# Kernel optimization log

Hardware: AMD Instinct MI355X
Metric: run time of the kernel (lower is better)

## Reference

```python
import jax, jax.numpy as jnp
import numpy as np

B, H, W, C = 8, 256, 256, 64
M1, M2 = 32, 32
SCALE = 1.0 / (C * C)


def setup_inputs() -> dict:
    key = jax.random.key(0)
    ku, k1, k2, k3, k4 = jax.random.split(key, 5)
    u = jax.random.normal(ku, (B, H, W, C), dtype=jnp.float32)
    wshape = (C, C, M1, M2)
    w_pos_r = SCALE * jax.random.normal(k1, wshape, dtype=jnp.float32)
    w_pos_i = SCALE * jax.random.normal(k2, wshape, dtype=jnp.float32)
    w_neg_r = SCALE * jax.random.normal(k3, wshape, dtype=jnp.float32)
    w_neg_i = SCALE * jax.random.normal(k4, wshape, dtype=jnp.float32)
    return {"u": u, "w_pos_r": w_pos_r, "w_pos_i": w_pos_i,
            "w_neg_r": w_neg_r, "w_neg_i": w_neg_i}


def _compl_mul2d(inp, weights):
    # inp: [B, m1, m2, Cin] complex; weights: [Cin, Cout, m1, m2] complex
    return jnp.einsum('bxyi,ioxy->bxyo', inp, weights)


def reference(u, w_pos_r, w_pos_i, w_neg_r, w_neg_i):
    b, h, w, c = u.shape
    wf = w // 2 + 1  # rfft size along W
    u_ft = jnp.fft.rfft2(u, axes=(1, 2))  # [B, H, Wf, C] complex
    w_pos = jax.lax.complex(w_pos_r, w_pos_i)
    w_neg = jax.lax.complex(w_neg_r, w_neg_i)
    top = _compl_mul2d(u_ft[:, :M1, :M2, :], w_pos)   # low positive freqs
    bot = _compl_mul2d(u_ft[:, h - M1:, :M2, :], w_neg)  # low negative freqs
    # out_ft zero-initialized, only truncated modes populated.
    # (Original allocates [B,H,W,C] but irfft2 with s=(H,W) only reads
    #  the first W//2+1 columns, which equals this [B,H,Wf,C] tensor.)
    out_ft = jnp.zeros((b, h, wf, c), dtype=u_ft.dtype)
    out_ft = out_ft.at[:, :M1, :M2, :].set(top)
    out_ft = out_ft.at[:, h - M1:, :M2, :].set(bot)
    # out_ft[:, -M1:M1] assignment in original is an empty slice (M1 <= H/2): no-op.
    return jnp.fft.irfft2(out_ft, s=(h, w), axes=(1, 2)).astype(u.dtype)
```

## Files before the change

kernel.cpp:

```cpp
#include <hip/hip_runtime.h>
#include <math.h>

#define BB 8
#define HH 256
#define WW 256
#define CC 64

__device__ inline void cmac(float2& a, float tx, float ty, float2 v) {
    a.x += tx * v.x - ty * v.y;
    a.y += tx * v.y + ty * v.x;
}

__global__ __launch_bounds__(256) void k_tw(float2* __restrict__ Tf,
                                            float2* __restrict__ Ti,
                                            float* __restrict__ Ty,
                                            float* __restrict__ T2) {
    int e = blockIdx.x * 256 + threadIdx.x;
    if (e < 16384) {
        int x = e >> 6;
        int j = e & 63;
        int kxa = j + ((j >> 5) * 192);
        int tt = (kxa * x) & 255;
        float ang = (float)tt * (6.283185307179586f / 256.0f);
        float s, c;
        sincosf(ang, &s, &c);
        Tf[(size_t)x * 64 + j] = make_float2(c, -s);
        const float k = 2.0f / 65536.0f;
        Ti[(size_t)j * 256 + x] = make_float2(c * k, s * k);
    } else {
        int f = e - 16384;
        if (f < 8192) {
            int yp = f >> 6;
            int col = f & 63;
            int par = (col >> 5) & 1;
            int cs = (col >> 4) & 1;
            int m = col & 15;
            int ky = 2 * m + par;
            int tt = (ky * yp) & 255;
            float ang = (float)tt * (6.283185307179586f / 256.0f);
            float s, c;
            sincosf(ang, &s, &c);
            Ty[f] = cs ? -s : c;
        } else {
            int g = f - 8192;
            int pi = g >> 12;
            int j = (g >> 7) & 31;
            int p = g & 127;
            int m = j >> 1, ri = j & 1;
            int ky = 2 * m + pi;
            int tt = (ky * p) & 255;
            float ang = (float)tt * (6.283185307179586f / 256.0f);
            float s, c;
            sincosf(ang, &s, &c);
            T2[g] = ri ? -s : c;
        }
    }
}

__global__ __launch_bounds__(256, 4) void k_fwd_y(const float* __restrict__ u,
                                                  const float* __restrict__ Ty,
                                                  float2* __restrict__ V) {
    __shared__ float ue[32 * 68];
    __shared__ float uo[32 * 68];
    __shared__ float Tt[32 * 68];

    int t = threadIdx.x;
    int b = blockIdx.x >> 8;
    int x = blockIdx.x & 255;
    int i4 = (t & 15) * 4;
    int w = t >> 4;
    int p = w & 1;
    int kyq = w >> 1;
    int yy = t >> 3;
    int c0 = (t & 7) * 8;

    const float* ub = u + ((size_t)(b * HH + x)) * (WW * CC);
    const float* uplane = p ? uo : ue;

    float ar0x=0,ar0y=0,ar0z=0,ar0w=0, ai0x=0,ai0y=0,ai0z=0,ai0w=0;
    float ar1x=0,ar1y=0,ar1z=0,ar1w=0, ai1x=0,ai1y=0,ai1z=0,ai1w=0;

    for (int yt = 0; yt < 4; ++yt) {
        const float* plo = ub + (size_t)(yt * 32 + yy) * CC + c0;
        const float* phi = plo + 128 * CC;
        float4 l0 = *(const float4*)(plo);
        float4 l1 = *(const float4*)(plo + 4);
        float4 h0 = *(const float4*)(phi);
        float4 h1 = *(const float4*)(phi + 4);
        const float* tsrc = Ty + (size_t)(yt * 32 + yy) * 64 + c0;
        float4 t0 = *(const float4*)(tsrc);
        float4 t1 = *(const float4*)(tsrc + 4);

        __syncthreads();
        int wb = yy * 68 + c0;
        *(float4*)(ue + wb)     = make_float4(l0.x + h0.x, l0.y + h0.y, l0.z + h0.z, l0.w + h0.w);
        *(float4*)(ue + wb + 4) = make_float4(l1.x + h1.x, l1.y + h1.y, l1.z + h1.z, l1.w + h1.w);
        *(float4*)(uo + wb)     = make_float4(l0.x - h0.x, l0.y - h0.y, l0.z - h0.z, l0.w - h0.w);
        *(float4*)(uo + wb + 4) = make_float4(l1.x - h1.x, l1.y - h1.y, l1.z - h1.z, l1.w - h1.w);
        *(float4*)(Tt + wb)     = t0;
        *(float4*)(Tt + wb + 4) = t1;
        __syncthreads();

        #pragma unroll
        for (int y2 = 0; y2 < 32; ++y2) {
            const float* tb = Tt + y2 * 68 + p * 32 + kyq * 2;
            float2 cp = *(const float2*)(tb);
            float2 sp = *(const float2*)(tb + 16);
            float4 uq = *(const float4*)(uplane + y2 * 68 + i4);
            ar0x += cp.x * uq.x; ar0y += cp.x * uq.y; ar0z += cp.x * uq.z; ar0w += cp.x * uq.w;
            ai0x += sp.x * uq.x; ai0y += sp.x * uq.y; ai0z += sp.x * uq.z; ai0w += sp.x * uq.w;
            ar1x += cp.y * uq.x; ar1y += cp.y * uq.y; ar1z += cp.y * uq.z; ar1w += cp.y * uq.w;
            ai1x += sp.y * uq.x; ai1y += sp.y * uq.y; ai1z += sp.y * uq.z; ai1w += sp.y * uq.w;
        }
    }

    {
        int ky = 4 * kyq + p;
        float2* vp = V + (size_t)(b * HH + x) * 2048 + ky * 64 + i4;
        *(float4*)(vp)     = make_float4(ar0x, ai0x, ar0y, ai0y);
        *(float4*)(vp + 2) = make_float4(ar0z, ai0z, ar0w, ai0w);
    }
    {
        int ky = 4 * kyq + 2 + p;
        float2* vp = V + (size_t)(b * HH + x) * 2048 + ky * 64 + i4;
        *(float4*)(vp)     = make_float4(ar1x, ai1x, ar1y, ai1y);
        *(float4*)(vp + 2) = make_float4(ar1z, ai1z, ar1w, ai1w);
    }
}

__global__ __launch_bounds__(256) void k_fwd_x(const float2* __restrict__ Tf,
                                               const float2* __restrict__ V,
                                               float2* __restrict__ U) {
    __shared__ float sRe[2 * 2048];
    __shared__ float sIm[2 * 2048];
    __shared__ float2 Ts[32 * 16];

    int bx = blockIdx.x;
    int jq = bx & 3;
    int ky = (bx >> 2) & 31;
    int b  = bx >> 7;
    int t = threadIdx.x;
    int jr = t >> 5;
    int ir = t & 31;

    float2 a00 = {0,0}, a01 = {0,0}, a10 = {0,0}, a11 = {0,0};

    const float2* vb = V + (size_t)b * (HH * 2048) + ky * 64;
    int vrow = t >> 3;
    int vcol = (t & 7) * 8;
    int tjj = (t & 7) * 2;
    int parOff = (jr & 1) * 2048;

    for (int x0 = 0; x0 < 128; x0 += 32) {
        const float2* plo = vb + (size_t)(x0 + vrow) * 2048 + vcol;
        const float2* phi = plo + 128 * 2048;
        float4 l0 = *(const float4*)(plo);
        float4 l1 = *(const float4*)(plo + 2);
        float4 l2 = *(const float4*)(plo + 4);
        float4 l3 = *(const float4*)(plo + 6);
        float4 h0 = *(const float4*)(phi);
        float4 h1 = *(const float4*)(phi + 2);
        float4 h2 = *(const float4*)(phi + 4);
        float4 h3 = *(const float4*)(phi + 6);
        float4 tv = *(const float4*)(Tf + (size_t)(x0 + vrow) * 64 + jq * 16 + tjj);

        __syncthreads();
        *(float4*)&Ts[vrow * 16 + tjj] = tv;
        int wb = vrow * 64 + vcol;
        *(float4*)(sRe + wb)            = make_float4(l0.x+h0.x, l0.z+h0.z, l1.x+h1.x, l1.z+h1.z);
        *(float4*)(sRe + wb + 4)        = make_float4(l2.x+h2.x, l2.z+h2.z, l3.x+h3.x, l3.z+h3.z);
        *(float4*)(sIm + wb)            = make_float4(l0.y+h0.y, l0.w+h0.w, l1.y+h1.y, l1.w+h1.w);
        *(float4*)(sIm + wb + 4)        = make_float4(l2.y+h2.y, l2.w+h2.w, l3.y+h3.y, l3.w+h3.w);
        *(float4*)(sRe + 2048 + wb)     = make_float4(l0.x-h0.x, l0.z-h0.z, l1.x-h1.x, l1.z-h1.z);
        *(float4*)(sRe + 2048 + wb + 4) = make_float4(l2.x-h2.x, l2.z-h2.z, l3.x-h3.x, l3.z-h3.z);
        *(float4*)(sIm + 2048 + wb)     = make_float4(l0.y-h0.y, l0.w-h0.w, l1.y-h1.y, l1.w-h1.w);
        *(float4*)(sIm + 2048 + wb + 4) = make_float4(l2.y-h2.y, l2.w-h2.w, l3.y-h3.y, l3.w-h3.w);
        __syncthreads();

        #pragma unroll
        for (int xx = 0; xx < 32; ++xx) {
            float2 t0 = Ts[xx * 16 + jr];
            float2 t1 = Ts[xx * 16 + jr + 8];
            const float* re = sRe + parOff + xx * 64;
            const float* im = sIm + parOff + xx * 64;
            float vr0 = re[ir], vr1 = re[ir + 32];
            float vi0 = im[ir], vi1 = im[ir + 32];
            a00.x += t0.x*vr0 - t0.y*vi0;  a00.y += t0.x*vi0 + t0.y*vr0;
            a01.x += t0.x*vr1 - t0.y*vi1;  a01.y += t0.x*vi1 + t0.y*vr1;
            a10.x += t1.x*vr0 - t1.y*vi0;  a10.y += t1.x*vi0 + t1.y*vr0;
            a11.x += t1.x*vr1 - t1.y*vi1;  a11.y += t1.x*vi1 + t1.y*vr1;
        }
    }

    int j0 = jq * 16 + jr;
    float2* u0 = U + ((size_t)(j0 * 32 + ky) * 8 + b) * 64 + ir;
    u0[0]  = a00;
    u0[32] = a01;
    float2* u1 = U + ((size_t)((j0 + 8) * 32 + ky) * 8 + b) * 64 + ir;
    u1[0]  = a10;
    u1[32] = a11;
}

__global__ __launch_bounds__(256) void k_modew(const float* __restrict__ wpr,
                                               const float* __restrict__ wpi,
                                               const float* __restrict__ wnr,
                                               const float* __restrict__ wni,
                                               const float2* __restrict__ U,
                                               float2* __restrict__ OF) {
    __shared__ float2 uS[4 * 8 * 64];
    __shared__ float2 wS[4 * 8 * 32];

    int bx = blockIdx.x;
    int j   = bx & 63;
    int kyt = (bx >> 6) & 7;
    int oh  = bx >> 9;
    int ky0 = kyt * 4;
    int sel = j >> 5, kxl = j & 31;
    const float* sr = sel ? wnr : wpr;
    const float* si = sel ? wni : wpi;
    int tid = threadIdx.x;

    const float2* up = U + (size_t)(j * 32 + ky0) * 512;
    #pragma unroll
    for (int k = 0; k < 8; ++k) uS[tid + 256 * k] = up[tid + 256 * k];

    int o32 = tid & 31;
    int bh  = tid >> 5;
    int irS = tid >> 5;
    int ooS = tid & 31;

    float2 acc[4];
    #pragma unroll
    for (int k = 0; k < 4; ++k) acc[k] = make_float2(0.f, 0.f);

    for (int it = 0; it < 8; ++it) {
        __syncthreads();
        {
            int ig = it * 8 + irS;
            int og = oh * 32 + ooS;
            size_t base = (((size_t)(ig * 64 + og)) * 32 + kxl) * 32 + ky0;
            float4 r0 = *(const float4*)(sr + base);
            float4 q0 = *(const float4*)(si + base);
            float2* wrow = wS + irS * 32 + ooS;
            wrow[0 * 256] = make_float2(r0.x, q0.x);
            wrow[1 * 256] = make_float2(r0.y, q0.y);
            wrow[2 * 256] = make_float2(r0.z, q0.z);
            wrow[3 * 256] = make_float2(r0.w, q0.w);
        }
        __syncthreads();
        #pragma unroll
        for (int ir = 0; ir < 8; ++ir) {
            int ig = it * 8 + ir;
            #pragma unroll
            for (int ky = 0; ky < 4; ++ky) {
                float2 wv = wS[ky * 256 + ir * 32 + o32];
                float2 uv = uS[ky * 512 + bh * 64 + ig];
                acc[ky].x += uv.x * wv.x - uv.y * wv.y;
                acc[ky].y += uv.x * wv.y + uv.y * wv.x;
            }
        }
    }

    int og = oh * 32 + o32;
    #pragma unroll
    for (int ky = 0; ky < 4; ++ky) {
        OF[((size_t)(bh * 32 + ky0 + ky) * 64 + j) * 64 + og] = acc[ky];
    }
}

__global__ __launch_bounds__(256) void k_inv_x(const float2* __restrict__ Ti,
                                               const float2* __restrict__ OF,
                                               float2* __restrict__ A) {
    __shared__ float2 Ts[32 * 32];
    __shared__ float2 Os[32 * 64];

    int bx = blockIdx.x;
    int xt = bx & 3;
    int ky = (bx >> 2) & 31;
    int b  = bx >> 7;
    int t = threadIdx.x;
    int or_ = t & 15;
    int xr = t >> 4;

    float2 acc[2][2][4];
    #pragma unroll
    for (int pa = 0; pa < 2; ++pa)
        #pragma unroll
        for (int p = 0; p < 2; ++p)
            #pragma unroll
            for (int q = 0; q < 4; ++q) acc[pa][p][q] = make_float2(0.f, 0.f);

    const float2* ofb = OF + (size_t)(b * 32 + ky) * 4096;
    int sj = t >> 3;
    int sx = (t & 7) * 4;
    int so = (t & 7) * 8;

    for (int kh = 0; kh < 2; ++kh) {
        const float2* tsrc = Ti + (size_t)(kh * 32 + sj) * 256 + xt * 32 + sx;
        float4 t0 = *(const float4*)(tsrc);
        float4 t1 = *(const float4*)(tsrc + 2);
        const float2* osrc = ofb + (size_t)(kh * 32 + sj) * 64 + so;
        float4 o0 = *(const float4*)(osrc);
        float4 o1 = *(const float4*)(osrc + 2);
        float4 o2 = *(const float4*)(osrc + 4);
        float4 o3 = *(const float4*)(osrc + 6);

        __syncthreads();
        *(float4*)&Ts[sj * 32 + sx]     = t0;
        *(float4*)&Ts[sj * 32 + sx + 2] = t1;
        float2* od = &Os[sj * 64 + so];
        *(float4*)(od)     = o0;
        *(float4*)(od + 2) = o1;
        *(float4*)(od + 4) = o2;
        *(float4*)(od + 6) = o3;
        __syncthreads();

        #pragma unroll
        for (int jj = 0; jj < 32; ++jj) {
            float4 tp = *(const float4*)&Ts[jj * 32 + xr * 2];
            float2 q0 = Os[jj * 64 + or_];
            float2 q1 = Os[jj * 64 + or_ + 16];
            float2 q2 = Os[jj * 64 + or_ + 32];
            float2 q3 = Os[jj * 64 + or_ + 48];
            const int pa = jj & 1;
            cmac(acc[pa][0][0], tp.x, tp.y, q0);
            cmac(acc[pa][0][1], tp.x, tp.y, q1);
            cmac(acc[pa][0][2], tp.x, tp.y, q2);
            cmac(acc[pa][0][3], tp.x, tp.y, q3);
            cmac(acc[pa][1][0], tp.z, tp.w, q0);
            cmac(acc[pa][1][1], tp.z, tp.w, q1);
            cmac(acc[pa][1][2], tp.z, tp.w, q2);
            cmac(acc[pa][1][3], tp.z, tp.w, q3);
        }
    }

    float sc = (ky == 0) ? 0.5f : 1.0f;
    #pragma unroll
    for (int p = 0; p < 2; ++p) {
        int x = xt * 32 + xr * 2 + p;
        float2* alo = A + ((size_t)(b * 256 + x) * 32 + ky) * 64 + or_;
        float2* ahi = A + ((size_t)(b * 256 + x + 128) * 32 + ky) * 64 + or_;
        #pragma unroll
        for (int q = 0; q < 4; ++q) {
            float2 se = acc[0][p][q], so2 = acc[1][p][q];
            alo[16 * q] = make_float2((se.x + so2.x) * sc, (se.y + so2.y) * sc);
            ahi[16 * q] = make_float2((se.x - so2.x) * sc, (se.y - so2.y) * sc);
        }
    }
}

__global__ __launch_bounds__(512, 2) void k_inv_y(const float* __restrict__ T2g,
                                                  const float2* __restrict__ A,
                                                  float* __restrict__ out) {
    __shared__ float As[2 * 32 * 68];
    __shared__ float T2s[2 * 32 * 132];

    int t = threadIdx.x;
    int b = blockIdx.x >> 8;
    int x = blockIdx.x & 255;
    int o4 = (t & 15) * 4;
    int pr = t >> 4;

    float acc[2][4][4];
    #pragma unroll
    for (int pi = 0; pi < 2; ++pi)
        #pragma unroll
        for (int pp = 0; pp < 4; ++pp)
            #pragma unroll
            for (int k = 0; k < 4; ++k) acc[pi][pp][k] = 0.f;

    {
        int ky = t >> 4;
        int oc = (t & 15) * 4;
        const float2* ap = A + (size_t)(b * 256 + x) * 2048 + ky * 64 + oc;
        float4 g0 = *(const float4*)(ap);
        float4 g1 = *(const float4*)(ap + 2);
        int pi = ky & 1, m = ky >> 1;
        float* re = As + ((pi * 32) + 2 * m) * 68 + oc;
        float* im = As + ((pi * 32) + 2 * m + 1) * 68 + oc;
        *(float4*)(re) = make_float4(g0.x, g0.z, g1.x, g1.z);
        *(float4*)(im) = make_float4(g0.y, g0.w, g1.y, g1.w);
    }
    {
        int row = t >> 3;
        int c = (t & 7) * 16;
        const float* tg = T2g + (size_t)row * 128 + c;
        float4 q0 = *(const float4*)(tg);
        float4 q1 = *(const float4*)(tg + 4);
        float4 q2 = *(const float4*)(tg + 8);
        float4 q3 = *(const float4*)(tg + 12);
        float* td = T2s + row * 132 + c;
        *(float4*)(td)      = q0;
        *(float4*)(td + 4)  = q1;
        *(float4*)(td + 8)  = q2;
        *(float4*)(td + 12) = q3;
    }
    __syncthreads();

    #pragma unroll
    for (int pi = 0; pi < 2; ++pi) {
        #pragma unroll
        for (int jj = 0; jj < 32; ++jj) {
            float4 ta = *(const float4*)(T2s + (pi * 32 + jj) * 132 + pr * 4);
            float4 av = *(const float4*)(As + (pi * 32 + jj) * 68 + o4);
            acc[pi][0][0] += ta.x * av.x;  acc[pi][0][1] += ta.x * av.y;
            acc[pi][0][2] += ta.x * av.z;  acc[pi][0][3] += ta.x * av.w;
            acc[pi][1][0] += ta.y * av.x;  acc[pi][1][1] += ta.y * av.y;
            acc[pi][1][2] += ta.y * av.z;  acc[pi][1][3] += ta.y * av.w;
            acc[pi][2][0] += ta.z * av.x;  acc[pi][2][1] += ta.z * av.y;
            acc[pi][2][2] += ta.z * av.z;  acc[pi][2][3] += ta.z * av.w;
            acc[pi][3][0] += ta.w * av.x;  acc[pi][3][1] += ta.w * av.y;
            acc[pi][3][2] += ta.w * av.z;  acc[pi][3][3] += ta.w * av.w;
        }
    }

    float* op = out + (size_t)(b * 256 + x) * (256 * 64);
    #pragma unroll
    for (int pp = 0; pp < 4; ++pp) {
        int p = pr * 4 + pp;
        float4 lo = make_float4(acc[0][pp][0] + acc[1][pp][0],
                                acc[0][pp][1] + acc[1][pp][1],
                                acc[0][pp][2] + acc[1][pp][2],
                                acc[0][pp][3] + acc[1][pp][3]);
        float4 hi = make_float4(acc[0][pp][0] - acc[1][pp][0],
                                acc[0][pp][1] - acc[1][pp][1],
                                acc[0][pp][2] - acc[1][pp][2],
                                acc[0][pp][3] - acc[1][pp][3]);
        *(float4*)(op + (size_t)p * 64 + o4)         = lo;
        *(float4*)(op + (size_t)(p + 128) * 64 + o4) = hi;
    }
}

extern "C" void kernel_launch(void* const* d_in, const int* in_sizes, int n_in,
                              void* d_out, int out_size, void* d_ws, size_t ws_size,
                              hipStream_t stream) {
    const float* u   = (const float*)d_in[0];
    const float* wpr = (const float*)d_in[1];
    const float* wpi = (const float*)d_in[2];
    const float* wnr = (const float*)d_in[3];
    const float* wni = (const float*)d_in[4];
    float* out = (float*)d_out;

    char* ws = (char*)d_ws;
    float2* U  = (float2*)(ws);
    float2* OF = (float2*)(ws + 8388608);
    float2* V  = (float2*)(ws + 16777216);
    float2* A  = V;
    float2* Tf = (float2*)(ws + 50331648);
    float2* Ti = (float2*)(ws + 50331648 + 131072);
    float*  Ty = (float*)(ws + 50331648 + 262144);
    float*  T2 = (float*)(ws + 50331648 + 262144 + 32768);

    k_tw<<<128, 256, 0, stream>>>(Tf, Ti, Ty, T2);
    k_fwd_y<<<BB * HH, 256, 0, stream>>>(u, Ty, V);
    k_fwd_x<<<1024, 256, 0, stream>>>(Tf, V, U);
    k_modew<<<1024, 256, 0, stream>>>(wpr, wpi, wnr, wni, U, OF);
    k_inv_x<<<1024, 256, 0, stream>>>(Ti, OF, A);
    k_inv_y<<<BB * HH, 512, 0, stream>>>(T2, A, out);
}
```

Baseline: 224.3 us.

## Enlarge per-thread tiles in forward y-DFT and retile mode-weight contraction

The forward y-direction DFT kernel drops to 128 threads per block, with each thread computing 8 channels instead of 4. This doubles register reuse of the twiddle values per shared-memory load. The mode-weight kernel is restructured: each block covers 8 output channels across all 32 ky modes, keeps U and W as split real/imag planes in padded shared memory, and has each thread accumulate 8 ky modes using vectorized LDS reads. The aim is less redundant weight and U traffic and fewer shared-memory loads per multiply, at the cost of higher register pressure and a smaller grid (512 blocks).

```diff
diff --git a/kernel.cpp b/kernel.cpp
--- a/kernel.cpp
+++ b/kernel.cpp
@@ -9,6 +9,9 @@
 __device__ inline void cmac(float2& a, float tx, float ty, float2 v) {
     a.x += tx * v.x - ty * v.y;
     a.y += tx * v.y + ty * v.x;
+}
+__device__ inline void fma4(float4& a, float s, float4 v) {
+    a.x += s * v.x; a.y += s * v.y; a.z += s * v.z; a.w += s * v.w;
 }
 
 __global__ __launch_bounds__(256) void k_tw(float2* __restrict__ Tf,
@@ -57,7 +60,7 @@
     }
 }
 
-__global__ __launch_bounds__(256, 4) void k_fwd_y(const float* __restrict__ u,
+__global__ __launch_bounds__(128, 3) void k_fwd_y(const float* __restrict__ u,
                                                   const float* __restrict__ Ty,
                                                   float2* __restrict__ V) {
     __shared__ float ue[32 * 68];
@@ -67,38 +70,52 @@
     int t = threadIdx.x;
     int b = blockIdx.x >> 8;
     int x = blockIdx.x & 255;
-    int i4 = (t & 15) * 4;
-    int w = t >> 4;
+    int i8 = (t & 7) * 8;
+    int w = t >> 3;
     int p = w & 1;
     int kyq = w >> 1;
-    int yy = t >> 3;
-    int c0 = (t & 7) * 8;
+    int yy = t >> 2;
+    int c0 = (t & 3) * 16;
 
     const float* ub = u + ((size_t)(b * HH + x)) * (WW * CC);
     const float* uplane = p ? uo : ue;
 
-    float ar0x=0,ar0y=0,ar0z=0,ar0w=0, ai0x=0,ai0y=0,ai0z=0,ai0w=0;
-    float ar1x=0,ar1y=0,ar1z=0,ar1w=0, ai1x=0,ai1y=0,ai1z=0,ai1w=0;
+    float4 A0r = {0,0,0,0}, A0i = {0,0,0,0};
+    float4 B0r = {0,0,0,0}, B0i = {0,0,0,0};
+    float4 A1r = {0,0,0,0}, A1i = {0,0,0,0};
+    float4 B1r = {0,0,0,0}, B1i = {0,0,0,0};
 
     for (int yt = 0; yt < 4; ++yt) {
         const float* plo = ub + (size_t)(yt * 32 + yy) * CC + c0;
         const float* phi = plo + 128 * CC;
         float4 l0 = *(const float4*)(plo);
         float4 l1 = *(const float4*)(plo + 4);
+        float4 l2 = *(const float4*)(plo + 8);
+        float4 l3 = *(const float4*)(plo + 12);
         float4 h0 = *(const float4*)(phi);
         float4 h1 = *(const float4*)(phi + 4);
+        float4 h2 = *(const float4*)(phi + 8);
+        float4 h3 = *(const float4*)(phi + 12);
         const float* tsrc = Ty + (size_t)(yt * 32 + yy) * 64 + c0;
         float4 t0 = *(const float4*)(tsrc);
         float4 t1 = *(const float4*)(tsrc + 4);
+        float4 t2 = *(const float4*)(tsrc + 8);
+        float4 t3 = *(const float4*)(tsrc + 12);
 
         __syncthreads();
         int wb = yy * 68 + c0;
-        *(float4*)(ue + wb)     = make_float4(l0.x + h0.x, l0.y + h0.y, l0.z + h0.z, l0.w + h0.w);
-        *(float4*)(ue + wb + 4) = make_float4(l1.x + h1.x, l1.y + h1.y, l1.z + h1.z, l1.w + h1.w);
-        *(float4*)(uo + wb)     = make_float4(l0.x - h0.x, l0.y - h0.y, l0.z - h0.z, l0.w - h0.w);
-        *(float4*)(uo + wb + 4) = make_float4(l1.x - h1.x, l1.y - h1.y, l1.z - h1.z, l1.w - h1.w);
-        *(float4*)(Tt + wb)     = t0;
-        *(float4*)(Tt + wb + 4) = t1;
+        *(float4*)(ue + wb)      = make_float4(l0.x+h0.x, l0.y+h0.y, l0.z+h0.z, l0.w+h0.w);
+        *(float4*)(ue + wb + 4)  = make_float4(l1.x+h1.x, l1.y+h1.y, l1.z+h1.z, l1.w+h1.w);
+        *(float4*)(ue + wb + 8)  = make_float4(l2.x+h2.x, l2.y+h2.y, l2.z+h2.z, l2.w+h2.w);
+        *(float4*)(ue + wb + 12) = make_float4(l3.x+h3.x, l3.y+h3.y, l3.z+h3.z, l3.w+h3.w);
+        *(float4*)(uo + wb)      = make_float4(l0.x-h0.x, l0.y-h0.y, l0.z-h0.z, l0.w-h0.w);
+        *(float4*)(uo + wb + 4)  = make_float4(l1.x-h1.x, l1.y-h1.y, l1.z-h1.z, l1.w-h1.w);
+        *(float4*)(uo + wb + 8)  = make_float4(l2.x-h2.x, l2.y-h2.y, l2.z-h2.z, l2.w-h2.w);
+        *(float4*)(uo + wb + 12) = make_float4(l3.x-h3.x, l3.y-h3.y, l3.z-h3.z, l3.w-h3.w);
+        *(float4*)(Tt + wb)      = t0;
+        *(float4*)(Tt + wb + 4)  = t1;
+        *(float4*)(Tt + wb + 8)  = t2;
+        *(float4*)(Tt + wb + 12) = t3;
         __syncthreads();
 
         #pragma unroll
@@ -106,25 +123,31 @@
             const float* tb = Tt + y2 * 68 + p * 32 + kyq * 2;
             float2 cp = *(const float2*)(tb);
             float2 sp = *(const float2*)(tb + 16);
-            float4 uq = *(const float4*)(uplane + y2 * 68 + i4);
-            ar0x += cp.x * uq.x; ar0y += cp.x * uq.y; ar0z += cp.x * uq.z; ar0w += cp.x * uq.w;
-            ai0x += sp.x * uq.x; ai0y += sp.x * uq.y; ai0z += sp.x * uq.z; ai0w += sp.x * uq.w;
-            ar1x += cp.y * uq.x; ar1y += cp.y * uq.y; ar1z += cp.y * uq.z; ar1w += cp.y * uq.w;
-            ai1x += sp.y * uq.x; ai1y += sp.y * uq.y; ai1z += sp.y * uq.z; ai1w += sp.y * uq.w;
+            const float* up = uplane + y2 * 68 + i8;
+            float4 uq0 = *(const float4*)(up);
+            float4 uq1 = *(const float4*)(up + 4);
+            fma4(A0r, cp.x, uq0);  fma4(A0i, sp.x, uq0);
+            fma4(B0r, cp.x, uq1);  fma4(B0i, sp.x, uq1);
+            fma4(A1r, cp.y, uq0);  fma4(A1i, sp.y, uq0);
+            fma4(B1r, cp.y, uq1);  fma4(B1i, sp.y, uq1);
         }
     }
 
     {
         int ky = 4 * kyq + p;
-        float2* vp = V + (size_t)(b * HH + x) * 2048 + ky * 64 + i4;
-        *(float4*)(vp)     = make_float4(ar0x, ai0x, ar0y, ai0y);
-        *(float4*)(vp + 2) = make_float4(ar0z, ai0z, ar0w, ai0w);
+        float2* vp = V + (size_t)(b * HH + x) * 2048 + ky * 64 + i8;
+        *(float4*)(vp)     = make_float4(A0r.x, A0i.x, A0r.y, A0i.y);
+        *(float4*)(vp + 2) = make_float4(A0r.z, A0i.z, A0r.w, A0i.w);
+        *(float4*)(vp + 4) = make_float4(B0r.x, B0i.x, B0r.y, B0i.y);
+        *(float4*)(vp + 6) = make_float4(B0r.z, B0i.z, B0r.w, B0i.w);
     }
     {
         int ky = 4 * kyq + 2 + p;
-        float2* vp = V + (size_t)(b * HH + x) * 2048 + ky * 64 + i4;
-        *(float4*)(vp)     = make_float4(ar1x, ai1x, ar1y, ai1y);
-        *(float4*)(vp + 2) = make_float4(ar1z, ai1z, ar1w, ai1w);
+        float2* vp = V + (size_t)(b * HH + x) * 2048 + ky * 64 + i8;
+        *(float4*)(vp)     = make_float4(A1r.x, A1i.x, A1r.y, A1i.y);
+        *(float4*)(vp + 2) = make_float4(A1r.z, A1i.z, A1r.w, A1i.w);
+        *(float4*)(vp + 4) = make_float4(B1r.x, B1i.x, B1r.y, B1i.y);
+        *(float4*)(vp + 6) = make_float4(B1r.z, B1i.z, B1r.w, B1i.w);
     }
 }
 
@@ -201,71 +224,104 @@
     u1[32] = a11;
 }
 
-__global__ __launch_bounds__(256) void k_modew(const float* __restrict__ wpr,
-                                               const float* __restrict__ wpi,
-                                               const float* __restrict__ wnr,
-                                               const float* __restrict__ wni,
-                                               const float2* __restrict__ U,
-                                               float2* __restrict__ OF) {
-    __shared__ float2 uS[4 * 8 * 64];
-    __shared__ float2 wS[4 * 8 * 32];
+__global__ __launch_bounds__(256, 2) void k_modew(const float* __restrict__ wpr,
+                                                  const float* __restrict__ wpi,
+                                                  const float* __restrict__ wnr,
+                                                  const float* __restrict__ wni,
+                                                  const float2* __restrict__ U,
+                                                  float2* __restrict__ OF) {
+    __shared__ float uRe[64 * 36];
+    __shared__ float uIm[64 * 36];
+    __shared__ float wRe[64 * 36];
+    __shared__ float wIm[64 * 36];
 
     int bx = blockIdx.x;
-    int j   = bx & 63;
-    int kyt = (bx >> 6) & 7;
-    int oh  = bx >> 9;
-    int ky0 = kyt * 4;
+    int j  = bx & 63;
+    int ot = bx >> 6;
     int sel = j >> 5, kxl = j & 31;
     const float* sr = sel ? wnr : wpr;
     const float* si = sel ? wni : wpi;
-    int tid = threadIdx.x;
-
-    const float2* up = U + (size_t)(j * 32 + ky0) * 512;
-    #pragma unroll
-    for (int k = 0; k < 8; ++k) uS[tid + 256 * k] = up[tid + 256 * k];
-
-    int o32 = tid & 31;
-    int bh  = tid >> 5;
-    int irS = tid >> 5;
-    int ooS = tid & 31;
-
-    float2 acc[4];
-    #pragma unroll
-    for (int k = 0; k < 4; ++k) acc[k] = make_float2(0.f, 0.f);
+    int t = threadIdx.x;
+    int og = t & 7;
+    int bh = (t >> 3) & 7;
+    int kk = t >> 6;
+    int sky = t >> 3;
+    int sb  = t & 7;
+    int wig = t >> 5;
+    int wog = (t >> 2) & 7;
+    int wc  = t & 3;
+
+    float2 acc0 = {0,0}, acc1 = {0,0}, acc2 = {0,0}, acc3 = {0,0};
+    float2 acc4 = {0,0}, acc5 = {0,0}, acc6 = {0,0}, acc7 = {0,0};
 
     for (int it = 0; it < 8; ++it) {
+        const float2* up = U + ((size_t)(j * 32 + sky) * 8 + sb) * 64 + it * 8;
+        float4 a0 = *(const float4*)(up);
+        float4 a1 = *(const float4*)(up + 2);
+        float4 a2 = *(const float4*)(up + 4);
+        float4 a3 = *(const float4*)(up + 6);
+        size_t wbase = (((size_t)((it * 8 + wig) * 64 + ot * 8 + wog)) * 32 + kxl) * 32 + wc * 8;
+        float4 r0 = *(const float4*)(sr + wbase);
+        float4 r1 = *(const float4*)(sr + wbase + 4);
+        float4 q0 = *(const float4*)(si + wbase);
+        float4 q1 = *(const float4*)(si + wbase + 4);
+
         __syncthreads();
         {
-            int ig = it * 8 + irS;
-            int og = oh * 32 + ooS;
-            size_t base = (((size_t)(ig * 64 + og)) * 32 + kxl) * 32 + ky0;
-            float4 r0 = *(const float4*)(sr + base);
-            float4 q0 = *(const float4*)(si + base);
-            float2* wrow = wS + irS * 32 + ooS;
-            wrow[0 * 256] = make_float2(r0.x, q0.x);
-            wrow[1 * 256] = make_float2(r0.y, q0.y);
-            wrow[2 * 256] = make_float2(r0.z, q0.z);
-            wrow[3 * 256] = make_float2(r0.w, q0.w);
-        }
-        __syncthreads();
-        #pragma unroll
-        for (int ir = 0; ir < 8; ++ir) {
-            int ig = it * 8 + ir;
-            #pragma unroll
-            for (int ky = 0; ky < 4; ++ky) {
-                float2 wv = wS[ky * 256 + ir * 32 + o32];
-                float2 uv = uS[ky * 512 + bh * 64 + ig];
-                acc[ky].x += uv.x * wv.x - uv.y * wv.y;
-                acc[ky].y += uv.x * wv.y + uv.y * wv.x;
-            }
-        }
-    }
-
-    int og = oh * 32 + o32;
-    #pragma unroll
-    for (int ky = 0; ky < 4; ++ky) {
-        OF[((size_t)(bh * 32 + ky0 + ky) * 64 + j) * 64 + og] = acc[ky];
-    }
+            float* urp = uRe + sb * 36 + sky;
+            float* uip = uIm + sb * 36 + sky;
+            urp[0*288] = a0.x;  uip[0*288] = a0.y;
+            urp[1*288] = a0.z;  uip[1*288] = a0.w;
+            urp[2*288] = a1.x;  uip[2*288] = a1.y;
+            urp[3*288] = a1.z;  uip[3*288] = a1.w;
+            urp[4*288] = a2.x;  uip[4*288] = a2.y;
+            urp[5*288] = a2.z;  uip[5*288] = a2.w;
+            urp[6*288] = a3.x;  uip[6*288] = a3.y;
+            urp[7*288] = a3.z;  uip[7*288] = a3.w;
+            float* wrp = wRe + (wig * 8 + wog) * 36 + wc * 8;
+            float* wip = wIm + (wig * 8 + wog) * 36 + wc * 8;
+            wrp[0] = r0.x; wrp[1] = r0.y; wrp[2] = r0.z; wrp[3] = r0.w;
+            wrp[4] = r1.x; wrp[5] = r1.y; wrp[6] = r1.z; wrp[7] = r1.w;
+            wip[0] = q0.x; wip[1] = q0.y; wip[2] = q0.z; wip[3] = q0.w;
+            wip[4] = q1.x; wip[5] = q1.y; wip[6] = q1.z; wip[7] = q1.w;
+        }
+        __syncthreads();
+
+        #pragma unroll
+        for (int i = 0; i < 8; ++i) {
+            const float* urp = uRe + (i * 8 + bh) * 36 + kk * 8;
+            float4 ur0 = *(const float4*)(urp);
+            float4 ur1 = *(const float4*)(urp + 4);
+            const float* uip = uIm + (i * 8 + bh) * 36 + kk * 8;
+            float4 ui0 = *(const float4*)(uip);
+            float4 ui1 = *(const float4*)(uip + 4);
+            const float* wrp = wRe + (i * 8 + og) * 36 + kk * 8;
+            float4 wr0 = *(const float4*)(wrp);
+            float4 wr1 = *(const float4*)(wrp + 4);
+            const float* wip = wIm + (i * 8 + og) * 36 + kk * 8;
+            float4 wi0 = *(const float4*)(wip);
+            float4 wi1 = *(const float4*)(wip + 4);
+            acc0.x += ur0.x*wr0.x - ui0.x*wi0.x;  acc0.y += ur0.x*wi0.x + ui0.x*wr0.x;
+            acc1.x += ur0.y*wr0.y - ui0.y*wi0.y;  acc1.y += ur0.y*wi0.y + ui0.y*wr0.y;
+            acc2.x += ur0.z*wr0.z - ui0.z*wi0.z;  acc2.y += ur0.z*wi0.z + ui0.z*wr0.z;
+            acc3.x += ur0.w*wr0.w - ui0.w*wi0.w;  acc3.y += ur0.w*wi0.w + ui0.w*wr0.w;
+            acc4.x += ur1.x*wr1.x - ui1.x*wi1.x;  acc4.y += ur1.x*wi1.x + ui1.x*wr1.x;
+            acc5.x += ur1.y*wr1.y - ui1.y*wi1.y;  acc5.y += ur1.y*wi1.y + ui1.y*wr1.y;
+            acc6.x += ur1.z*wr1.z - ui1.z*wi1.z;  acc6.y += ur1.z*wi1.z + ui1.z*wr1.z;
+            acc7.x += ur1.w*wr1.w - ui1.w*wi1.w;  acc7.y += ur1.w*wi1.w + ui1.w*wr1.w;
+        }
+    }
+
+    int ogg = ot * 8 + og;
+    int ky0 = kk * 8;
+    OF[((size_t)(bh * 32 + ky0 + 0) * 64 + j) * 64 + ogg] = acc0;
+    OF[((size_t)(bh * 32 + ky0 + 1) * 64 + j) * 64 + ogg] = acc1;
+    OF[((size_t)(bh * 32 + ky0 + 2) * 64 + j) * 64 + ogg] = acc2;
+    OF[((size_t)(bh * 32 + ky0 + 3) * 64 + j) * 64 + ogg] = acc3;
+    OF[((size_t)(bh * 32 + ky0 + 4) * 64 + j) * 64 + ogg] = acc4;
+    OF[((size_t)(bh * 32 + ky0 + 5) * 64 + j) * 64 + ogg] = acc5;
+    OF[((size_t)(bh * 32 + ky0 + 6) * 64 + j) * 64 + ogg] = acc6;
+    OF[((size_t)(bh * 32 + ky0 + 7) * 64 + j) * 64 + ogg] = acc7;
 }
 
 __global__ __launch_bounds__(256) void k_inv_x(const float2* __restrict__ Ti,
@@ -452,9 +508,9 @@
     float*  T2 = (float*)(ws + 50331648 + 262144 + 32768);
 
     k_tw<<<128, 256, 0, stream>>>(Tf, Ti, Ty, T2);
-    k_fwd_y<<<BB * HH, 256, 0, stream>>>(u, Ty, V);
+    k_fwd_y<<<BB * HH, 128, 0, stream>>>(u, Ty, V);
     k_fwd_x<<<1024, 256, 0, stream>>>(Tf, V, U);
-    k_modew<<<1024, 256, 0, stream>>>(wpr, wpi, wnr, wni, U, OF);
+    k_modew<<<512, 256, 0, stream>>>(wpr, wpi, wnr, wni, U, OF);
     k_inv_x<<<1024, 256, 0, stream>>>(Ti, OF, A);
     k_inv_y<<<BB * HH, 512, 0, stream>>>(T2, A, out);
 }
```

After: 272.1 us. 21.3% more time.
